# Kernel optimization log

Measured on AMD Instinct MI355X. Metric: run time of the kernel, lower is better.

The kernel has to match this reference:

```python
import jax, jax.numpy as jnp
import numpy as np

E, S, D, A, L, H, C = 8, 6000, 128, 16, 64, 256, 64
B = 50            # no_batches hardcoded in torch forward
T = S // B        # number of outer integration steps
DT = 0.5          # solver dt; t_horizon=[0,1] -> 2 reversible-Heun substeps
NSUB = 2
SQDT = float(np.sqrt(DT))


def setup_inputs():
    ks = jax.random.split(jax.random.key(0), 24)
    w = lambda k, shp, s=0.05: (jax.random.normal(k, shp) * s).astype(jnp.float32)
    z = lambda shp: jnp.zeros(shp, jnp.float32)
    return dict(
        xs=w(ks[0], (E, S, D), 1.0),
        actions=w(ks[1], (E, S, A), 1.0),
        z0_noise=w(ks[2], (T, E, B, L), 1.0),
        dW=w(ks[3], (T, NSUB, E * B, L), 1.0),
        enc_w1=w(ks[4], (E, D, H)), enc_b1=z((E, H)),
        enc_w2=w(ks[5], (E, H, C)), enc_b2=z((E, C)),
        qz0_w=w(ks[6], (E, C, 2 * L)), qz0_b=z((E, 2 * L)),
        act_w=w(ks[7], (E, L + A + D, L)), act_b=z((E, L)),
        fw1=w(ks[8], (L, H)), fb1=z((H,)),
        fw2=w(ks[9], (H, H)), fb2=z((H,)),
        fw3=w(ks[10], (H, L)), fb3=z((L,)),
        hw1=w(ks[11], (L, H)), hb1=z((H,)),
        hw2=w(ks[12], (H, H)), hb2=z((H,)),
        hw3=w(ks[13], (H, L)), hb3=z((L,)),
        gw1=w(ks[14], (L, H)), gb1=z((L, H)),
        gw2=w(ks[15], (L, H), 0.02), gb2=jnp.ones((L,), jnp.float32),
        pw1=w(ks[16], (E, L, H)), pb1=z((E, H)),
        pw2=w(ks[17], (E, H, H)), pb2=z((E, H)),
        pw3=w(ks[18], (E, H, D)), pb3=z((E, D)),
        pz0_mean=z((E, 1, L)), pz0_logstd=z((E, 1, L)),
    )


def reference(xs, actions, z0_noise, dW,
              enc_w1, enc_b1, enc_w2, enc_b2, qz0_w, qz0_b, act_w, act_b,
              fw1, fb1, fw2, fb2, fw3, fb3, hw1, hb1, hw2, hb2, hw3, hb3,
              gw1, gb1, gw2, gb2, pw1, pb1, pw2, pb2, pw3, pb3,
              pz0_mean, pz0_logstd):
    xs_r = xs.reshape(E, T, B, D).transpose(1, 0, 2, 3)       # [T,E,B,D]
    act_r = actions.reshape(E, T, B, A).transpose(1, 0, 2, 3)  # [T,E,B,A]

    def mlp3(y, w1, b1, w2, b2, w3, b3):
        h1 = jax.nn.sigmoid(y @ w1 + b1)
        h2 = jax.nn.sigmoid(h1 @ w2 + b2)
        return h2 @ w3 + b3

    def g_fn(y):  # per-latent-dim diagonal diffusion nets, vectorized over L
        hc = jax.nn.sigmoid(y[..., None] * gw1 + gb1)          # [N,L,H]
        return jnp.sum(hc * gw2, axis=-1) + gb2                # [N,L]

    def drift_all(zc):
        fz = mlp3(zc, fw1, fb1, fw2, fb2, fw3, fb3)
        hz = mlp3(zc, hw1, hb1, hw2, hb2, hw3, hb3)
        gz = g_fn(zc)
        u = (fz - hz) / gz
        return fz, gz, 0.5 * jnp.sum(u * u, axis=-1)           # logqp drift

    def sde_solve(zini, dWs):  # reversible Heun, Stratonovich, logqp-augmented
        zc = zh = zini
        lc = lh = jnp.zeros(zini.shape[0], zini.dtype)
        fz, gz, lf = drift_all(zc)
        for k in range(NSUB):
            dWk = dWs[k] * SQDT
            zh_n = 2.0 * zc - zh + fz * DT + gz * dWk
            lh_n = 2.0 * lc - lh + lf * DT
            fz1, gz1, lf1 = drift_all(zh_n)
            zc = zc + 0.5 * (fz + fz1) * DT + 0.5 * (gz + gz1) * dWk
            lc = lc + 0.5 * (lf + lf1) * DT
            zh, lh, fz, gz, lf = zh_n, lh_n, fz1, gz1, lf1
        return zc, lc

    def step(z_prev, inp):
        i, x_i, a_i, n_i, dW_i = inp
        c1 = jax.nn.sigmoid(jnp.einsum('ebd,edh->ebh', x_i, enc_w1) + enc_b1[:, None])
        ctx = jnp.einsum('ebh,ehc->ebc', c1, enc_w2) + enc_b2[:, None]
        q = jnp.einsum('ebc,eck->ebk', ctx, qz0_w) + qz0_b[:, None]
        qm, ql = q[..., :L], q[..., L:]
        z0 = qm + jnp.exp(ql) * n_i
        z_in = jnp.where(i == 0, z0, z_prev)
        lat = jnp.concatenate([z_in, a_i, x_i], axis=-1)
        z_enc = jnp.einsum('ebf,efl->ebl', lat, act_w) + act_b[:, None]
        zf, lr = sde_solve(z_enc.reshape(E * B, L), dW_i)
        z_new = zf.reshape(E, B, L)
        p1 = jax.nn.sigmoid(jnp.einsum('ebl,elh->ebh', z_new, pw1) + pb1[:, None])
        p2 = jax.nn.sigmoid(jnp.einsum('ebh,ehk->ebk', p1, pw2) + pb2[:, None])
        xm = jnp.einsum('ebh,ehd->ebd', p2, pw3) + pb3[:, None]
        # KL(q(z0) || p(z0)) elementwise, p has mean pz0_mean, logstd pz0_logstd
        kl = (pz0_logstd - ql
              + (jnp.exp(2.0 * ql) + (qm - pz0_mean) ** 2) / (2.0 * jnp.exp(2.0 * pz0_logstd))
              - 0.5)
        logqp0 = kl.sum(-1).mean(-1)  # [E]
        return z_new, (xm, lr.reshape(E, B), logqp0)

    z_init = jnp.zeros((E, B, L), xs.dtype)
    _, (xm_all, lr_all, lq0_all) = jax.lax.scan(
        step, z_init, (jnp.arange(T), xs_r, act_r, z0_noise, dW))
    predicted_xs = xm_all.transpose(1, 0, 2, 3).reshape(E, T * B, D)
    logqp_path = lr_all.mean(-1).sum(0) + lq0_all.sum(0)  # [E]
    return logqp_path, predicted_xs
```

## Files before the change

### kernel.cpp

```cpp
#include <hip/hip_runtime.h>
#include <math.h>

#define E 8
#define S 6000
#define D 128
#define A 16
#define L 64
#define H 256
#define C 64
#define B 50
#define T 120
#define NSUB 2
#define FLAT 208
#define RTOT 400
#define RPB 10
#define NBLK (RTOT / RPB)
#define BGRP 10
#define NBG 5

#define DT 0.5f
#define SQDT 0.70710678118654752440f

#define GNT 4096
#define GYMIN (-128.0f)
#define GDY 0.0625f
#define GINVDY 16.0f

typedef __attribute__((ext_vector_type(8))) short bf16x8;
typedef __attribute__((ext_vector_type(4))) float f32x4;

#define MFMA16(a, b, c) __builtin_amdgcn_mfma_f32_16x16x32_bf16(a, b, c, 0, 0, 0)

__device__ __forceinline__ float sigf(float x) { return 1.0f / (1.0f + __expf(-x)); }

__device__ __forceinline__ unsigned short f2bf(float x) {
    union { float f; unsigned u; } v; v.f = x;
    unsigned r = (v.u + 0x7FFFu + ((v.u >> 16) & 1u)) >> 16;
    return (unsigned short)r;
}

__device__ __forceinline__ void bar_lgkm() {
    asm volatile("s_waitcnt lgkmcnt(0)" ::: "memory");
    __builtin_amdgcn_s_barrier();
    __builtin_amdgcn_sched_barrier(0);
}

__global__ void gtab_kernel(const float* __restrict__ gw1, const float* __restrict__ gb1,
                            const float* __restrict__ gw2, const float* __restrict__ gb2,
                            float* __restrict__ tab) {
    int idx = blockIdx.x * blockDim.x + threadIdx.x;
    if (idx >= L * GNT) return;
    int l = idx / GNT, i = idx % GNT;
    float y = GYMIN + (float)i * GDY;
    const float* w1 = gw1 + l * H;
    const float* b1 = gb1 + l * H;
    const float* w2 = gw2 + l * H;
    float acc = gb2[l];
    #pragma unroll 4
    for (int h = 0; h < H; ++h) acc += w2[h] * sigf(y * w1[h] + b1[h]);
    tab[idx] = acc;
}

__global__ void packB_kernel(const float* __restrict__ src, unsigned short* __restrict__ dst,
                             int K, int N) {
    int idx = blockIdx.x * 256 + threadIdx.x;
    if (idx >= K * N) return;
    int j = idx & 7;
    int lane = (idx >> 3) & 63;
    int t2 = idx >> 9;
    int KC = K >> 5;
    int kc = t2 % KC, n = t2 / KC;
    int k = (kc << 5) + ((lane >> 4) << 3) + j;
    int c = (n << 4) + (lane & 15);
    dst[idx] = f2bf(src[k * N + c]);
}

__global__ void packAW_kernel(const float* __restrict__ aw, unsigned short* __restrict__ dst) {
    int idx = blockIdx.x * 256 + threadIdx.x;
    if (idx >= E * L * L) return;
    int e = idx >> 12;
    int rem = idx & 4095;
    int j = rem & 7;
    int lane = (rem >> 3) & 63;
    int t2 = rem >> 9;
    int kc = t2 & 1, n = t2 >> 1;
    int k = (kc << 5) + ((lane >> 4) << 3) + j;
    int c = (n << 4) + (lane & 15);
    dst[idx] = f2bf(aw[((size_t)e * FLAT + k) * L + c]);
}

__global__ __launch_bounds__(256) void enc_kernel(const float* __restrict__ xs, const float* __restrict__ z0n,
                           const float* __restrict__ ew1, const float* __restrict__ eb1,
                           const float* __restrict__ ew2, const float* __restrict__ eb2,
                           const float* __restrict__ qw,  const float* __restrict__ qb,
                           const float* __restrict__ pm,  const float* __restrict__ pl,
                           float* __restrict__ z0buf, float* __restrict__ logqp0p) {
    int bid = blockIdx.x;
    int bg = bid % NBG; int te = bid / NBG; int e = te % E; int t = te / E;
    int tid = threadIdx.x;
    __shared__ float xsh[BGRP][D];
    __shared__ float c1s[BGRP][H];
    __shared__ float part[4][C][BGRP];
    __shared__ float ctxs[BGRP][C];
    __shared__ float qs[BGRP][2 * L];

    for (int i = tid; i < BGRP * D; i += 256) {
        int j = i / D, d = i % D;
        xsh[j][d] = xs[((size_t)e * S + (size_t)t * B + bg * BGRP + j) * D + d];
    }
    __syncthreads();
    {
        float bias = eb1[e * H + tid];
        float acc[BGRP];
        #pragma unroll
        for (int j = 0; j < BGRP; ++j) acc[j] = bias;
        const float* w = ew1 + (size_t)e * D * H + tid;
        #pragma unroll 4
        for (int d = 0; d < D; ++d) {
            float wv = w[(size_t)d * H];
            #pragma unroll
            for (int j = 0; j < BGRP; ++j) acc[j] += xsh[j][d] * wv;
        }
        #pragma unroll
        for (int j = 0; j < BGRP; ++j) c1s[j][tid] = sigf(acc[j]);
    }
    __syncthreads();
    {
        int c = tid & 63, kq = tid >> 6;
        float acc[BGRP];
        #pragma unroll
        for (int j = 0; j < BGRP; ++j) acc[j] = 0.f;
        const float* w = ew2 + (size_t)e * H * C + c;
        #pragma unroll 4
        for (int h = kq * 64; h < kq * 64 + 64; ++h) {
            float wv = w[(size_t)h * C];
            #pragma unroll
            for (int j = 0; j < BGRP; ++j) acc[j] += c1s[j][h] * wv;
        }
        #pragma unroll
        for (int j = 0; j < BGRP; ++j) part[kq][c][j] = acc[j];
    }
    __syncthreads();
    if (tid < C) {
        float bias = eb2[e * C + tid];
        #pragma unroll
        for (int j = 0; j < BGRP; ++j)
            ctxs[j][tid] = part[0][tid][j] + part[1][tid][j] + part[2][tid][j] + part[3][tid][j] + bias;
    }
    __syncthreads();
    if (tid < 2 * L) {
        float bias = qb[e * 2 * L + tid];
        float acc[BGRP];
        #pragma unroll
        for (int j = 0; j < BGRP; ++j) acc[j] = bias;
        const float* w = qw + (size_t)e * C * 2 * L + tid;
        #pragma unroll 4
        for (int c = 0; c < C; ++c) {
            float wv = w[(size_t)c * 2 * L];
            #pragma unroll
            for (int j = 0; j < BGRP; ++j) acc[j] += ctxs[j][c] * wv;
        }
        #pragma unroll
        for (int j = 0; j < BGRP; ++j) qs[j][tid] = acc[j];
    }
    __syncthreads();
    if (tid < L) {
        int l = tid;
        float kacc = 0.f;
        float m = pm[e * L + l], ls = pl[e * L + l];
        float inv2e = 1.0f / (2.0f * __expf(2.0f * ls));
        #pragma unroll
        for (int j = 0; j < BGRP; ++j) {
            float qm = qs[j][l], ql = qs[j][L + l];
            if (t == 0) {
                int b = bg * BGRP + j;
                float n = z0n[((size_t)e * B + b) * L + l];
                z0buf[((size_t)e * B + b) * L + l] = qm + __expf(ql) * n;
            }
            float dq = qm - m;
            kacc += ls - ql + (__expf(2.f * ql) + dq * dq) * inv2e - 0.5f;
        }
        #pragma unroll
        for (int off = 32; off; off >>= 1) kacc += __shfl_xor(kacc, off);
        if (l == 0) logqp0p[bid] = kacc / (float)B;
    }
}

__global__ __launch_bounds__(64) void ax_kernel(const float* __restrict__ xs, const float* __restrict__ actions,
                          const float* __restrict__ aw, const float* __restrict__ ab,
                          float* __restrict__ ax) {
    int bid = blockIdx.x;
    int bg = bid % NBG; int te = bid / NBG; int e = te % E; int t = te / E;
    int tid = threadIdx.x;
    __shared__ float xrow[BGRP][D];
    __shared__ float arow[BGRP][A];
    for (int i = tid; i < BGRP * D; i += 64) {
        int j = i / D, d = i % D;
        xrow[j][d] = xs[((size_t)e * S + (size_t)t * B + bg * BGRP + j) * D + d];
    }
    for (int i = tid; i < BGRP * A; i += 64) {
        int j = i / A, a = i % A;
        arow[j][a] = actions[((size_t)e * S + (size_t)t * B + bg * BGRP + j) * A + a];
    }
    __syncthreads();
    int l = tid;
    float acc[BGRP];
    float bias = ab[e * L + l];
    #pragma unroll
    for (int j = 0; j < BGRP; ++j) acc[j] = bias;
    const float* awp = aw + ((size_t)e * FLAT + L) * L + l;
    #pragma unroll 4
    for (int a = 0; a < A; ++a) {
        float wv = awp[(size_t)a * L];
        #pragma unroll
        for (int j = 0; j < BGRP; ++j) acc[j] += arow[j][a] * wv;
    }
    const float* xwp = aw + ((size_t)e * FLAT + L + A) * L + l;
    #pragma unroll 4
    for (int d = 0; d < D; ++d) {
        float wv = xwp[(size_t)d * L];
        #pragma unroll
        for (int j = 0; j < BGRP; ++j) acc[j] += xrow[j][d] * wv;
    }
    size_t rbase = (size_t)t * RTOT + e * B + bg * BGRP;
    #pragma unroll
    for (int j = 0; j < BGRP; ++j) ax[(rbase + j) * L + l] = acc[j];
}

__global__ __launch_bounds__(1024, 4) void seq_kernel(
    const unsigned short* __restrict__ pkAW, const float* __restrict__ dW,
    const float* __restrict__ z0buf, const float* __restrict__ axbuf,
    const unsigned short* __restrict__ pk1, const unsigned short* __restrict__ pk2,
    const unsigned short* __restrict__ pk3,
    const float* __restrict__ fb1, const float* __restrict__ hb1,
    const float* __restrict__ fb2, const float* __restrict__ hb2,
    const float* __restrict__ fb3, const float* __restrict__ hb3,
    const float* __restrict__ gtab, float* __restrict__ z_all, float* __restrict__ rowlr)
{
    __shared__ __align__(16) bf16x8 w1L[4096];
    __shared__ __align__(16) unsigned short ybfA[1024];
    __shared__ __align__(16) unsigned short ybfZ[1024];
    __shared__ __align__(16) unsigned short o1[2][4096];
    __shared__ __align__(16) unsigned short o2[2][4096];
    __shared__ float fh2[2][2][16][64];
    __shared__ float zcS[16][64];

    int tid = threadIdx.x;
    int wv = tid >> 6;
    int lane = tid & 63;
    int rA = lane & 15, kg = lane >> 4;
    int sw = (rA & 7) << 3;
    int r_base = blockIdx.x * RPB;
    int e = blockIdx.x / 5;

    for (int i = tid; i < 4096; i += 1024) w1L[i] = ((const bf16x8*)pk1)[i];

    int net = wv >> 3;
    int na = (wv & 7) << 1;
    int cnet = wv >> 3, crem = wv & 7, n0c = crem >> 1, khc = crem & 1;
    int nZ = wv & 3;
    int lZ = (nZ << 4) + rA;

    bf16x8 W0r0 = {}, W0r1 = {}, W2r[16], W3r[4];
    if (wv < 4) {
        const bf16x8* p0 = (const bf16x8*)pkAW + (e << 9);
        W0r0 = p0[(nZ * 2 + 0) * 64 + lane];
        W0r1 = p0[(nZ * 2 + 1) * 64 + lane];
    }
    {
        const bf16x8* p2 = (const bf16x8*)pk2 + net * 8192;
        #pragma unroll
        for (int i2 = 0; i2 < 2; ++i2)
            #pragma unroll
            for (int kc = 0; kc < 8; ++kc)
                W2r[i2 * 8 + kc] = p2[((na + i2) * 8 + kc) * 64 + lane];
        const bf16x8* p3 = (const bf16x8*)pk3 + cnet * 2048;
        #pragma unroll
        for (int kc = 0; kc < 4; ++kc)
            W3r[kc] = p3[(n0c * 8 + khc * 4 + kc) * 64 + lane];
    }
    float biasA0, biasA1, biasB0, biasB1, biasC;
    {
        const float* b1 = net ? hb1 : fb1;
        const float* b2 = net ? hb2 : fb2;
        const float* b3 = cnet ? hb3 : fb3;
        biasA0 = b1[((na + 0) << 4) + rA];
        biasA1 = b1[((na + 1) << 4) + rA];
        biasB0 = b2[((na + 0) << 4) + rA];
        biasB1 = b2[((na + 1) << 4) + rA];
        biasC = khc ? 0.f : b3[(n0c << 4) + rA];
    }

    int orow = tid >> 6, ol = tid & 63;
    bool owner = (tid < RPB * L);
    float zc_r = 0.f, zh_r = 0.f, fz_r = 0.f, gz_r = 1.f;
    float dwA_r = 0.f, dwB_r = 0.f;
    float gt0 = 1.f, gt1 = 1.f, gfr = 0.f;
    float scal = 0.f;

    {
        int r = tid >> 6;
        float v = (tid < RPB * L) ? z0buf[(size_t)r_base * L + tid] : 0.f;
        ybfZ[tid ^ ((r & 7) << 3)] = f2bf(v);
    }
    __syncthreads();

    auto gprep = [&](float v) {
        float x = (v - GYMIN) * GINVDY;
        x = fminf(fmaxf(x, 0.0f), (float)(GNT - 2) + 0.999f);
        int ii = (int)x;
        gfr = x - (float)ii;
        const float* tl = gtab + ((size_t)ol << 12);
        gt0 = tl[ii];
        gt1 = tl[ii + 1];
    };

    for (int t = 0; t < T; ++t) {
        if (wv < 4) {
            float axv[4];
            #pragma unroll
            for (int rr = 0; rr < 4; ++rr) {
                int r = (kg << 2) + rr;
                axv[rr] = (r < RPB) ? axbuf[((size_t)t * RTOT + r_base + r) * L + lZ] : 0.f;
            }
            bf16x8 Z0 = *(const bf16x8*)&ybfZ[((rA << 6) + (kg << 3)) ^ sw];
            bf16x8 Z1 = *(const bf16x8*)&ybfZ[((rA << 6) + 32 + (kg << 3)) ^ sw];
            f32x4 acc = (f32x4){0.f, 0.f, 0.f, 0.f};
            acc = MFMA16(Z0, W0r0, acc);
            acc = MFMA16(Z1, W0r1, acc);
            #pragma unroll
            for (int rr = 0; rr < 4; ++rr) {
                int r = (kg << 2) + rr;
                float v = acc[rr] + axv[rr];
                zcS[r][lZ] = v;
                ybfA[((r << 6) + lZ) ^ ((r & 7) << 3)] = f2bf(v);
            }
        }
        bar_lgkm();

        #pragma unroll
        for (int d = 0; d < 3; ++d) {
            if (d == 0 && owner) {
                zc_r = zcS[orow][ol];
                zh_r = zc_r;
                gprep(zc_r);
                dwA_r = dW[((size_t)(2 * t) * RTOT + r_base + orow) * L + ol] * SQDT;
                dwB_r = dW[((size_t)(2 * t + 1) * RTOT + r_base + orow) * L + ol] * SQDT;
            }
            {
                bf16x8 A0 = *(const bf16x8*)&ybfA[((rA << 6) + (kg << 3)) ^ sw];
                bf16x8 A1 = *(const bf16x8*)&ybfA[((rA << 6) + 32 + (kg << 3)) ^ sw];
                f32x4 acc0 = (f32x4){biasA0, biasA0, biasA0, biasA0};
                f32x4 acc1 = (f32x4){biasA1, biasA1, biasA1, biasA1};
                acc0 = MFMA16(A0, w1L[net * 2048 + ((na + 0) * 2 + 0) * 64 + lane], acc0);
                acc0 = MFMA16(A1, w1L[net * 2048 + ((na + 0) * 2 + 1) * 64 + lane], acc0);
                acc1 = MFMA16(A0, w1L[net * 2048 + ((na + 1) * 2 + 0) * 64 + lane], acc1);
                acc1 = MFMA16(A1, w1L[net * 2048 + ((na + 1) * 2 + 1) * 64 + lane], acc1);
                unsigned short* o1n = o1[net];
                int c0 = ((na + 0) << 4) + rA;
                int c1 = ((na + 1) << 4) + rA;
                #pragma unroll
                for (int rr = 0; rr < 4; ++rr) {
                    int r = (kg << 2) + rr;
                    int rx = (r & 7) << 3;
                    o1n[((r << 8) + c0) ^ rx] = f2bf(sigf(acc0[rr]));
                    o1n[((r << 8) + c1) ^ rx] = f2bf(sigf(acc1[rr]));
                }
            }
            bar_lgkm();
            {
                const unsigned short* o1n = o1[net];
                f32x4 acc0 = (f32x4){biasB0, biasB0, biasB0, biasB0};
                f32x4 acc1 = (f32x4){biasB1, biasB1, biasB1, biasB1};
                #pragma unroll
                for (int kc = 0; kc < 8; ++kc) {
                    bf16x8 Ak = *(const bf16x8*)&o1n[((rA << 8) + (kc << 5) + (kg << 3)) ^ sw];
                    acc0 = MFMA16(Ak, W2r[kc], acc0);
                    acc1 = MFMA16(Ak, W2r[8 + kc], acc1);
                }
                unsigned short* o2n = o2[net];
                int c0 = ((na + 0) << 4) + rA;
                int c1 = ((na + 1) << 4) + rA;
                #pragma unroll
                for (int rr = 0; rr < 4; ++rr) {
                    int r = (kg << 2) + rr;
                    int rx = (r & 7) << 3;
                    o2n[((r << 8) + c0) ^ rx] = f2bf(sigf(acc0[rr]));
                    o2n[((r << 8) + c1) ^ rx] = f2bf(sigf(acc1[rr]));
                }
            }
            bar_lgkm();
            {
                const unsigned short* o2n = o2[cnet];
                f32x4 acc = (f32x4){biasC, biasC, biasC, biasC};
                #pragma unroll
                for (int kc = 0; kc < 4; ++kc) {
                    bf16x8 Ak = *(const bf16x8*)&o2n[((rA << 8) + (((khc << 2) + kc) << 5) + (kg << 3)) ^ sw];
                    acc = MFMA16(Ak, W3r[kc], acc);
                }
                int c = (n0c << 4) + rA;
                #pragma unroll
                for (int rr = 0; rr < 4; ++rr)
                    fh2[cnet][khc][(kg << 2) + rr][c] = acc[rr];
            }
            bar_lgkm();
            if (owner) {
                float fv = fh2[0][0][orow][ol] + fh2[0][1][orow][ol];
                float hv = fh2[1][0][orow][ol] + fh2[1][1][orow][ol];
                float gv = gt0 * (1.0f - gfr) + gt1 * gfr;
                float uu = (fv - hv) / gv;
                float us = uu * uu;
                if (d == 0) {
                    scal += us;
                    fz_r = fv; gz_r = gv;
                    float y1 = zc_r + fv * DT + gv * dwA_r;
                    zh_r = y1;
                    ybfA[tid ^ ((orow & 7) << 3)] = f2bf(y1);
                    gprep(y1);
                } else if (d == 1) {
                    zc_r += 0.5f * (fz_r + fv) * DT + 0.5f * (gz_r + gv) * dwA_r;
                    scal += 2.0f * us;
                    float y2 = 2.f * zc_r - zh_r + fv * DT + gv * dwB_r;
                    fz_r = fv; gz_r = gv;
                    ybfA[tid ^ ((orow & 7) << 3)] = f2bf(y2);
                    gprep(y2);
                } else {
                    zc_r += 0.5f * (fz_r + fv) * DT + 0.5f * (gz_r + gv) * dwB_r;
                    scal += us;
                    z_all[((size_t)t * RTOT + r_base) * L + tid] = zc_r;
                    ybfZ[tid ^ ((orow & 7) << 3)] = f2bf(zc_r);
                }
            }
            bar_lgkm();
        }
    }
    if (owner) {
        float s = scal;
        #pragma unroll
        for (int off = 32; off; off >>= 1) s += __shfl_xor(s, off);
        if (ol == 0) rowlr[r_base + orow] = 0.25f * DT * s;
    }
}

__global__ __launch_bounds__(256) void proj_kernel(const float* __restrict__ z_all,
                            const float* __restrict__ pw1, const float* __restrict__ pb1,
                            const float* __restrict__ pw2, const float* __restrict__ pb2,
                            const float* __restrict__ pw3, const float* __restrict__ pb3,
                            float* __restrict__ out) {
    int bid = blockIdx.x;
    int bg = bid % NBG; int te = bid / NBG; int e = te % E; int t = te / E;
    int tid = threadIdx.x;
    __shared__ float zs[BGRP][L];
    __shared__ float p1s[BGRP][H];
    __shared__ float p2s[BGRP][H];
    __shared__ float part3[D][BGRP];
    size_t rbase = (size_t)t * RTOT + e * B + bg * BGRP;
    for (int i = tid; i < BGRP * L; i += 256) {
        int j = i >> 6, ll = i & 63;
        zs[j][ll] = z_all[(rbase + j) * L + ll];
    }
    __syncthreads();
    {
        float bias = pb1[e * H + tid];
        float acc[BGRP];
        #pragma unroll
        for (int j = 0; j < BGRP; ++j) acc[j] = bias;
        const float* w = pw1 + (size_t)e * L * H + tid;
        #pragma unroll 4
        for (int k = 0; k < L; ++k) {
            float wv = w[(size_t)k * H];
            #pragma unroll
            for (int j = 0; j < BGRP; ++j) acc[j] += zs[j][k] * wv;
        }
        #pragma unroll
        for (int j = 0; j < BGRP; ++j) p1s[j][tid] = sigf(acc[j]);
    }
    __syncthreads();
    {
        float bias = pb2[e * H + tid];
        float acc[BGRP];
        #pragma unroll
        for (int j = 0; j < BGRP; ++j) acc[j] = bias;
        const float* w = pw2 + (size_t)e * H * H + tid;
        #pragma unroll 4
        for (int k = 0; k < H; ++k) {
            float wv = w[(size_t)k * H];
            #pragma unroll
            for (int j = 0; j < BGRP; ++j) acc[j] += p1s[j][k] * wv;
        }
        #pragma unroll
        for (int j = 0; j < BGRP; ++j) p2s[j][tid] = sigf(acc[j]);
    }
    __syncthreads();
    float acc3[BGRP];
    {
        int dd = tid & 127, kh = tid >> 7;
        #pragma unroll
        for (int j = 0; j < BGRP; ++j) acc3[j] = 0.f;
        const float* w = pw3 + (size_t)e * H * D + dd;
        #pragma unroll 4
        for (int k = kh * 128; k < kh * 128 + 128; ++k) {
            float wv = w[(size_t)k * D];
            #pragma unroll
            for (int j = 0; j < BGRP; ++j) acc3[j] += p2s[j][k] * wv;
        }
        if (kh == 1) {
            #pragma unroll
            for (int j = 0; j < BGRP; ++j) part3[dd][j] = acc3[j];
        }
    }
    __syncthreads();
    if (tid < D) {
        float bias = pb3[e * D + tid];
        #pragma unroll
        for (int j = 0; j < BGRP; ++j) {
            out[8 + ((size_t)e * S + (size_t)t * B + bg * BGRP + j) * D + tid]
                = acc3[j] + part3[tid][j] + bias;
        }
    }
}

__global__ void fin_kernel(const float* __restrict__ logqp0p, const float* __restrict__ rowlr,
                           float* __restrict__ out) {
    int e = threadIdx.x;
    if (e < E) {
        float acc = 0.f;
        for (int t = 0; t < T; ++t)
            for (int bg = 0; bg < NBG; ++bg)
                acc += logqp0p[(t * E + e) * NBG + bg];
        float s = 0.f;
        for (int b = 0; b < B; ++b) s += rowlr[e * B + b];
        out[e] = acc + s / (float)B;
    }
}

extern "C" void kernel_launch(void* const* d_in, const int* in_sizes, int n_in,
                              void* d_out, int out_size, void* d_ws, size_t ws_size,
                              hipStream_t stream) {
    const float* xs      = (const float*)d_in[0];
    const float* actions = (const float*)d_in[1];
    const float* z0n     = (const float*)d_in[2];
    const float* dWp     = (const float*)d_in[3];
    const float* ew1     = (const float*)d_in[4];
    const float* eb1     = (const float*)d_in[5];
    const float* ew2     = (const float*)d_in[6];
    const float* eb2     = (const float*)d_in[7];
    const float* qw      = (const float*)d_in[8];
    const float* qb      = (const float*)d_in[9];
    const float* aw      = (const float*)d_in[10];
    const float* ab      = (const float*)d_in[11];
    const float* fw1     = (const float*)d_in[12];
    const float* fb1     = (const float*)d_in[13];
    const float* fw2     = (const float*)d_in[14];
    const float* fb2     = (const float*)d_in[15];
    const float* fw3     = (const float*)d_in[16];
    const float* fb3     = (const float*)d_in[17];
    const float* hw1     = (const float*)d_in[18];
    const float* hb1     = (const float*)d_in[19];
    const float* hw2     = (const float*)d_in[20];
    const float* hb2     = (const float*)d_in[21];
    const float* hw3     = (const float*)d_in[22];
    const float* hb3     = (const float*)d_in[23];
    const float* gw1     = (const float*)d_in[24];
    const float* gb1     = (const float*)d_in[25];
    const float* gw2     = (const float*)d_in[26];
    const float* gb2     = (const float*)d_in[27];
    const float* pw1     = (const float*)d_in[28];
    const float* pb1     = (const float*)d_in[29];
    const float* pw2     = (const float*)d_in[30];
    const float* pb2     = (const float*)d_in[31];
    const float* pw3     = (const float*)d_in[32];
    const float* pb3     = (const float*)d_in[33];
    const float* pm      = (const float*)d_in[34];
    const float* pl      = (const float*)d_in[35];

    float* ws      = (float*)d_ws;
    float* z0buf   = ws;
    float* axbuf   = z0buf + 25600;
    float* z_all   = axbuf + 3072000;
    float* logqp0p = z_all + 3072000;
    float* rowlr   = logqp0p + 4800;
    float* gtab    = rowlr + 400;
    unsigned short* pku = (unsigned short*)(gtab + 262144);
    unsigned short* pk1 = pku;
    unsigned short* pk2 = pk1 + 32768;
    unsigned short* pk3 = pk2 + 131072;
    unsigned short* pkAW = pk3 + 32768;
    float* out     = (float*)d_out;

    packB_kernel<<<64,  256, 0, stream>>>(fw1, pk1,          64, 256);
    packB_kernel<<<64,  256, 0, stream>>>(hw1, pk1 + 16384,  64, 256);
    packB_kernel<<<256, 256, 0, stream>>>(fw2, pk2,          256, 256);
    packB_kernel<<<256, 256, 0, stream>>>(hw2, pk2 + 65536,  256, 256);
    packB_kernel<<<64,  256, 0, stream>>>(fw3, pk3,          256, 64);
    packB_kernel<<<64,  256, 0, stream>>>(hw3, pk3 + 16384,  256, 64);
    packAW_kernel<<<128, 256, 0, stream>>>(aw, pkAW);
    gtab_kernel<<<1024, 256, 0, stream>>>(gw1, gb1, gw2, gb2, gtab);
    enc_kernel<<<T * E * NBG, 256, 0, stream>>>(xs, z0n, ew1, eb1, ew2, eb2, qw, qb, pm, pl, z0buf, logqp0p);
    ax_kernel<<<T * E * NBG, 64, 0, stream>>>(xs, actions, aw, ab, axbuf);
    seq_kernel<<<NBLK, 1024, 0, stream>>>(pkAW, dWp, z0buf, axbuf,
                                          pk1, pk2, pk3,
                                          fb1, hb1, fb2, hb2, fb3, hb3,
                                          gtab, z_all, rowlr);
    proj_kernel<<<T * E * NBG, 256, 0, stream>>>(z_all, pw1, pb1, pw2, pb2, pw3, pb3, out);
    fin_kernel<<<1, 64, 0, stream>>>(logqp0p, rowlr, out);
}
```

Measured before the change: 3.107 ms.

## Vectorize LDS stores via lane transposes, split MFMA chains, cheapen sigmoid and bf16 rounding

```diff
diff --git a/kernel.cpp b/kernel.cpp
--- a/kernel.cpp
+++ b/kernel.cpp
@@ -31,18 +31,42 @@
 
 #define MFMA16(a, b, c) __builtin_amdgcn_mfma_f32_16x16x32_bf16(a, b, c, 0, 0, 0)
 
-__device__ __forceinline__ float sigf(float x) { return 1.0f / (1.0f + __expf(-x)); }
+__device__ __forceinline__ float sigf(float x) {
+    return __builtin_amdgcn_rcpf(1.0f + __expf(-x));
+}
 
 __device__ __forceinline__ unsigned short f2bf(float x) {
     union { float f; unsigned u; } v; v.f = x;
-    unsigned r = (v.u + 0x7FFFu + ((v.u >> 16) & 1u)) >> 16;
-    return (unsigned short)r;
+    return (unsigned short)((v.u + 0x8000u) >> 16);
+}
+
+__device__ __forceinline__ uint2 pack4(float v0, float v1, float v2, float v3) {
+    uint2 w;
+    w.x = (unsigned)f2bf(v0) | ((unsigned)f2bf(v1) << 16);
+    w.y = (unsigned)f2bf(v2) | ((unsigned)f2bf(v3) << 16);
+    return w;
+}
+
+__device__ __forceinline__ void xpose4(float& a0, float& a1, float& a2, float& a3, int m) {
+    float x0 = __shfl_xor(a0, 2), x1 = __shfl_xor(a1, 2);
+    float x2 = __shfl_xor(a2, 2), x3 = __shfl_xor(a3, 2);
+    bool hi = (m & 2);
+    float b0 = hi ? x2 : a0;
+    float b1 = hi ? x3 : a1;
+    float b2 = hi ? a2 : x0;
+    float b3 = hi ? a3 : x1;
+    float y0 = __shfl_xor(b0, 1), y1 = __shfl_xor(b1, 1);
+    float y2 = __shfl_xor(b2, 1), y3 = __shfl_xor(b3, 1);
+    bool od = (m & 1);
+    a0 = od ? y1 : b0;
+    a1 = od ? b1 : y0;
+    a2 = od ? y3 : b2;
+    a3 = od ? b3 : y2;
 }
 
 __device__ __forceinline__ void bar_lgkm() {
     asm volatile("s_waitcnt lgkmcnt(0)" ::: "memory");
     __builtin_amdgcn_s_barrier();
-    __builtin_amdgcn_sched_barrier(0);
 }
 
 __global__ void gtab_kernel(const float* __restrict__ gw1, const float* __restrict__ gb1,
@@ -57,7 +81,7 @@
     const float* w2 = gw2 + l * H;
     float acc = gb2[l];
     #pragma unroll 4
-    for (int h = 0; h < H; ++h) acc += w2[h] * sigf(y * w1[h] + b1[h]);
+    for (int h = 0; h < H; ++h) acc += w2[h] * (1.0f / (1.0f + __expf(-(y * w1[h] + b1[h]))));
     tab[idx] = acc;
 }
 
@@ -72,7 +96,8 @@
     int kc = t2 % KC, n = t2 / KC;
     int k = (kc << 5) + ((lane >> 4) << 3) + j;
     int c = (n << 4) + (lane & 15);
-    dst[idx] = f2bf(src[k * N + c]);
+    union { float f; unsigned u; } v; v.f = src[k * N + c];
+    dst[idx] = (unsigned short)((v.u + 0x7FFFu + ((v.u >> 16) & 1u)) >> 16);
 }
 
 __global__ void packAW_kernel(const float* __restrict__ aw, unsigned short* __restrict__ dst) {
@@ -86,7 +111,8 @@
     int kc = t2 & 1, n = t2 >> 1;
     int k = (kc << 5) + ((lane >> 4) << 3) + j;
     int c = (n << 4) + (lane & 15);
-    dst[idx] = f2bf(aw[((size_t)e * FLAT + k) * L + c]);
+    union { float f; unsigned u; } v; v.f = aw[((size_t)e * FLAT + k) * L + c];
+    dst[idx] = (unsigned short)((v.u + 0x7FFFu + ((v.u >> 16) & 1u)) >> 16);
 }
 
 __global__ __launch_bounds__(256) void enc_kernel(const float* __restrict__ xs, const float* __restrict__ z0n,
@@ -227,7 +253,7 @@
     for (int j = 0; j < BGRP; ++j) ax[(rbase + j) * L + l] = acc[j];
 }
 
-__global__ __launch_bounds__(1024, 4) void seq_kernel(
+__global__ __launch_bounds__(1024, 1) void seq_kernel(
     const unsigned short* __restrict__ pkAW, const float* __restrict__ dW,
     const float* __restrict__ z0buf, const float* __restrict__ axbuf,
     const unsigned short* __restrict__ pk1, const unsigned short* __restrict__ pk2,
@@ -242,13 +268,14 @@
     __shared__ __align__(16) unsigned short ybfZ[1024];
     __shared__ __align__(16) unsigned short o1[2][4096];
     __shared__ __align__(16) unsigned short o2[2][4096];
-    __shared__ float fh2[2][2][16][64];
-    __shared__ float zcS[16][64];
+    __shared__ __align__(16) float fhF[4096];
+    __shared__ __align__(16) float zcF[1024];
 
     int tid = threadIdx.x;
     int wv = tid >> 6;
     int lane = tid & 63;
     int rA = lane & 15, kg = lane >> 4;
+    int m4 = lane & 3, rAhi = (lane >> 2) & 3;
     int sw = (rA & 7) << 3;
     int r_base = blockIdx.x * RPB;
     int e = blockIdx.x / 5;
@@ -293,6 +320,7 @@
 
     int orow = tid >> 6, ol = tid & 63;
     bool owner = (tid < RPB * L);
+    int oswz = ((orow << 6) + ol) ^ ((orow & 7) << 2);
     float zc_r = 0.f, zh_r = 0.f, fz_r = 0.f, gz_r = 1.f;
     float dwA_r = 0.f, dwB_r = 0.f;
     float gt0 = 1.f, gt1 = 1.f, gfr = 0.f;
@@ -328,20 +356,20 @@
             f32x4 acc = (f32x4){0.f, 0.f, 0.f, 0.f};
             acc = MFMA16(Z0, W0r0, acc);
             acc = MFMA16(Z1, W0r1, acc);
-            #pragma unroll
-            for (int rr = 0; rr < 4; ++rr) {
-                int r = (kg << 2) + rr;
-                float v = acc[rr] + axv[rr];
-                zcS[r][lZ] = v;
-                ybfA[((r << 6) + lZ) ^ ((r & 7) << 3)] = f2bf(v);
-            }
+            float v0 = acc[0] + axv[0], v1 = acc[1] + axv[1];
+            float v2 = acc[2] + axv[2], v3 = acc[3] + axv[3];
+            xpose4(v0, v1, v2, v3, m4);
+            int r = (kg << 2) + m4;
+            int cb = (nZ << 4) + (rAhi << 2);
+            *(f32x4*)&zcF[((r << 6) + cb) ^ ((r & 7) << 2)] = (f32x4){v0, v1, v2, v3};
+            *(uint2*)&ybfA[((r << 6) + cb) ^ ((r & 7) << 3)] = pack4(v0, v1, v2, v3);
         }
         bar_lgkm();
 
         #pragma unroll
         for (int d = 0; d < 3; ++d) {
             if (d == 0 && owner) {
-                zc_r = zcS[orow][ol];
+                zc_r = zcF[oswz];
                 zh_r = zc_r;
                 gprep(zc_r);
                 dwA_r = dW[((size_t)(2 * t) * RTOT + r_base + orow) * L + ol] * SQDT;
@@ -357,14 +385,14 @@
                 acc1 = MFMA16(A0, w1L[net * 2048 + ((na + 1) * 2 + 0) * 64 + lane], acc1);
                 acc1 = MFMA16(A1, w1L[net * 2048 + ((na + 1) * 2 + 1) * 64 + lane], acc1);
                 unsigned short* o1n = o1[net];
-                int c0 = ((na + 0) << 4) + rA;
-                int c1 = ((na + 1) << 4) + rA;
+                int r = (kg << 2) + m4;
                 #pragma unroll
-                for (int rr = 0; rr < 4; ++rr) {
-                    int r = (kg << 2) + rr;
-                    int rx = (r & 7) << 3;
-                    o1n[((r << 8) + c0) ^ rx] = f2bf(sigf(acc0[rr]));
-                    o1n[((r << 8) + c1) ^ rx] = f2bf(sigf(acc1[rr]));
+                for (int i2 = 0; i2 < 2; ++i2) {
+                    f32x4 a = i2 ? acc1 : acc0;
+                    float s0 = sigf(a[0]), s1 = sigf(a[1]), s2 = sigf(a[2]), s3 = sigf(a[3]);
+                    xpose4(s0, s1, s2, s3, m4);
+                    int cb = ((na + i2) << 4) + (rAhi << 2);
+                    *(uint2*)&o1n[((r << 8) + cb) ^ ((r & 7) << 3)] = pack4(s0, s1, s2, s3);
                 }
             }
             bar_lgkm();
@@ -372,41 +400,60 @@
                 const unsigned short* o1n = o1[net];
                 f32x4 acc0 = (f32x4){biasB0, biasB0, biasB0, biasB0};
                 f32x4 acc1 = (f32x4){biasB1, biasB1, biasB1, biasB1};
+                f32x4 acc0b = (f32x4){0.f, 0.f, 0.f, 0.f};
+                f32x4 acc1b = (f32x4){0.f, 0.f, 0.f, 0.f};
                 #pragma unroll
-                for (int kc = 0; kc < 8; ++kc) {
+                for (int kc = 0; kc < 4; ++kc) {
                     bf16x8 Ak = *(const bf16x8*)&o1n[((rA << 8) + (kc << 5) + (kg << 3)) ^ sw];
                     acc0 = MFMA16(Ak, W2r[kc], acc0);
                     acc1 = MFMA16(Ak, W2r[8 + kc], acc1);
                 }
+                #pragma unroll
+                for (int kc = 4; kc < 8; ++kc) {
+                    bf16x8 Ak = *(const bf16x8*)&o1n[((rA << 8) + (kc << 5) + (kg << 3)) ^ sw];
+                    acc0b = MFMA16(Ak, W2r[kc], acc0b);
+                    acc1b = MFMA16(Ak, W2r[8 + kc], acc1b);
+                }
                 unsigned short* o2n = o2[net];
-                int c0 = ((na + 0) << 4) + rA;
-                int c1 = ((na + 1) << 4) + rA;
+                int r = (kg << 2) + m4;
                 #pragma unroll
-                for (int rr = 0; rr < 4; ++rr) {
-                    int r = (kg << 2) + rr;
-                    int rx = (r & 7) << 3;
-                    o2n[((r << 8) + c0) ^ rx] = f2bf(sigf(acc0[rr]));
-                    o2n[((r << 8) + c1) ^ rx] = f2bf(sigf(acc1[rr]));
+                for (int i2 = 0; i2 < 2; ++i2) {
+                    f32x4 a = i2 ? acc1 : acc0;
+                    f32x4 b = i2 ? acc1b : acc0b;
+                    float s0 = sigf(a[0] + b[0]), s1 = sigf(a[1] + b[1]);
+                    float s2 = sigf(a[2] + b[2]), s3 = sigf(a[3] + b[3]);
+                    xpose4(s0, s1, s2, s3, m4);
+                    int cb = ((na + i2) << 4) + (rAhi << 2);
+                    *(uint2*)&o2n[((r << 8) + cb) ^ ((r & 7) << 3)] = pack4(s0, s1, s2, s3);
                 }
             }
             bar_lgkm();
             {
                 const unsigned short* o2n = o2[cnet];
                 f32x4 acc = (f32x4){biasC, biasC, biasC, biasC};
-                #pragma unroll
-                for (int kc = 0; kc < 4; ++kc) {
-                    bf16x8 Ak = *(const bf16x8*)&o2n[((rA << 8) + (((khc << 2) + kc) << 5) + (kg << 3)) ^ sw];
-                    acc = MFMA16(Ak, W3r[kc], acc);
+                f32x4 accb = (f32x4){0.f, 0.f, 0.f, 0.f};
+                {
+                    bf16x8 Ak0 = *(const bf16x8*)&o2n[((rA << 8) + (((khc << 2) + 0) << 5) + (kg << 3)) ^ sw];
+                    bf16x8 Ak1 = *(const bf16x8*)&o2n[((rA << 8) + (((khc << 2) + 1) << 5) + (kg << 3)) ^ sw];
+                    bf16x8 Ak2 = *(const bf16x8*)&o2n[((rA << 8) + (((khc << 2) + 2) << 5) + (kg << 3)) ^ sw];
+                    bf16x8 Ak3 = *(const bf16x8*)&o2n[((rA << 8) + (((khc << 2) + 3) << 5) + (kg << 3)) ^ sw];
+                    acc  = MFMA16(Ak0, W3r[0], acc);
+                    accb = MFMA16(Ak1, W3r[1], accb);
+                    acc  = MFMA16(Ak2, W3r[2], acc);
+                    accb = MFMA16(Ak3, W3r[3], accb);
                 }
-                int c = (n0c << 4) + rA;
-                #pragma unroll
-                for (int rr = 0; rr < 4; ++rr)
-                    fh2[cnet][khc][(kg << 2) + rr][c] = acc[rr];
+                float v0 = acc[0] + accb[0], v1 = acc[1] + accb[1];
+                float v2 = acc[2] + accb[2], v3 = acc[3] + accb[3];
+                xpose4(v0, v1, v2, v3, m4);
+                int r = (kg << 2) + m4;
+                int cb = (n0c << 4) + (rAhi << 2);
+                *(f32x4*)&fhF[(((cnet << 1) + khc) << 10) + (((r << 6) + cb) ^ ((r & 7) << 2))]
+                    = (f32x4){v0, v1, v2, v3};
             }
             bar_lgkm();
             if (owner) {
-                float fv = fh2[0][0][orow][ol] + fh2[0][1][orow][ol];
-                float hv = fh2[1][0][orow][ol] + fh2[1][1][orow][ol];
+                float fv = fhF[oswz] + fhF[1024 + oswz];
+                float hv = fhF[2048 + oswz] + fhF[3072 + oswz];
                 float gv = gt0 * (1.0f - gfr) + gt1 * gfr;
                 float uu = (fv - hv) / gv;
                 float us = uu * uu;
```

After: 3.336 ms. 7.4% more time.
